# Kernel optimization log

Measured on AMD Instinct MI355X. Metric: run time of the kernel, lower is better.

## Reference

```python
import jax, jax.numpy as jnp
import numpy as np

B, S, D, H = 2, 4096, 1024, 16
DH = D // H  # 64


def setup_inputs() -> dict:
    key = jax.random.key(0)
    ks = jax.random.split(key, 5)
    x = jax.random.normal(ks[0], (B, S, D), dtype=jnp.float32)
    scale = 1.0 / np.sqrt(D)
    Wq = jax.random.normal(ks[1], (D, D), dtype=jnp.float32) * scale
    Wk = jax.random.normal(ks[2], (D, D), dtype=jnp.float32) * scale
    Wv = jax.random.normal(ks[3], (D, D), dtype=jnp.float32) * scale
    Wo = jax.random.normal(ks[4], (D, D), dtype=jnp.float32) * scale
    bo = jnp.zeros((D,), dtype=jnp.float32)
    return {"x": x, "Wq": Wq, "Wk": Wk, "Wv": Wv, "Wo": Wo, "bo": bo}


def reference(x, Wq, Wk, Wv, Wo, bo):
    b, s, d = x.shape
    # QKV projections (no bias), split heads: [b, s, H, DH]
    q = (x @ Wq).reshape(b, s, H, DH)
    k = (x @ Wk).reshape(b, s, H, DH)
    v = (x @ Wv).reshape(b, s, H, DH)
    # scores: [b, H, s, s]
    scores = jnp.einsum("bqhd,bkhd->bhqk", q, k)
    # causal mask: upper triangle (j > i) set to -inf, then scale by sqrt(d_head)
    causal = jnp.triu(jnp.ones((s, s), dtype=bool), k=1)
    scores = jnp.where(causal, -jnp.inf, scores)
    weights = jax.nn.softmax(scores / jnp.sqrt(jnp.float32(DH)), axis=-1)
    # dropout rate is 0.0 -> identity
    ctx = jnp.einsum("bhqk,bkhd->bqhd", weights, v).reshape(b, s, d)
    return ctx @ Wo + bo
```

## Files before the change

### kernel.cpp

```cpp
#include <hip/hip_runtime.h>
#include <hip/hip_bf16.h>
#include <stdint.h>
#include <math.h>

#define BATCH 2
#define S_LEN 4096
#define DMODEL 1024
#define NH 16
#define DHEAD 64
#define MTOK (BATCH * S_LEN)

#define QSCALE 0.1803368801111793f

typedef unsigned short u16;
typedef __attribute__((ext_vector_type(8))) short bf16x8;
typedef __attribute__((ext_vector_type(4))) float f32x4;
typedef __attribute__((ext_vector_type(16))) float f32x16;
typedef __attribute__((ext_vector_type(4))) unsigned short u16x4;

__device__ __forceinline__ float b2f(u16 u) {
  union { unsigned int i; float f; } v; v.i = ((unsigned int)u) << 16; return v.f;
}
__device__ __forceinline__ u16 f2b(float f) {
  union { float f; unsigned int i; } v; v.f = f;
  unsigned int r = v.i + 0x7FFF + ((v.i >> 16) & 1);
  return (u16)(r >> 16);
}
__device__ __forceinline__ unsigned int pk2(float hi, float lo) {
  union { float f; unsigned int u; } a, b; a.f = hi; b.f = lo;
  return __builtin_amdgcn_perm(a.u, b.u, 0x07060302u);
}
__device__ __forceinline__ void pswap(unsigned int& a, unsigned int& b) {
  asm("v_permlane32_swap_b32 %0, %1" : "+v"(a), "+v"(b));
}

__device__ __forceinline__ void gl_lds16(const u16* g, u16* l) {
  __builtin_amdgcn_global_load_lds(
      (__attribute__((address_space(1))) void*)(u16*)g,
      (__attribute__((address_space(3))) void*)l, 16, 0, 0);
}

__global__ void detect_dtype(const unsigned int* __restrict__ x, int* __restrict__ flag) {
  __shared__ int cnt;
  if (threadIdx.x == 0) cnt = 0;
  __syncthreads();
  int c = 0;
  for (int i = threadIdx.x; i < 4096; i += 256) {
    unsigned int w = x[i];
    int e = (w >> 7) & 0xFF;
    if (e >= 100 && e <= 135) c++;
  }
  atomicAdd(&cnt, c);
  __syncthreads();
  if (threadIdx.x == 0) *flag = (cnt > 2048) ? 1 : 0;
}

__global__ void convert_x(const void* __restrict__ xin, u16* __restrict__ xc,
                          const int* __restrict__ flagp) {
  const int isb = *flagp;
  long e = ((long)blockIdx.x * 256 + threadIdx.x) * 4;
  if (isb) {
    *(uint2*)&xc[e] = *(const uint2*)((const u16*)xin + e);
  } else {
    float4 f = *(const float4*)((const float*)xin + e);
    xc[e + 0] = f2b(f.x);
    xc[e + 1] = f2b(f.y);
    xc[e + 2] = f2b(f.z);
    xc[e + 3] = f2b(f.w);
  }
}

__global__ void transpose4(const void* __restrict__ W0, const void* __restrict__ W1,
                           const void* __restrict__ W2, const void* __restrict__ W3,
                           u16* __restrict__ out, const int* __restrict__ flagp) {
  __shared__ u16 tile[32][33];
  const int isb = *flagp;
  int z = blockIdx.z;
  const void* W = (z == 0) ? W0 : (z == 1) ? W1 : (z == 2) ? W2 : W3;
  u16* o = out + (long)z * (DMODEL * DMODEL);
  int x = blockIdx.x * 32 + threadIdx.x;
  int y0 = blockIdx.y * 32;
  if (isb) {
    const u16* Wb = (const u16*)W;
#pragma unroll
    for (int i = 0; i < 32; i += 8)
      tile[threadIdx.y + i][threadIdx.x] = Wb[(long)(y0 + threadIdx.y + i) * DMODEL + x];
  } else {
    const float* Wf = (const float*)W;
#pragma unroll
    for (int i = 0; i < 32; i += 8)
      tile[threadIdx.y + i][threadIdx.x] = f2b(Wf[(long)(y0 + threadIdx.y + i) * DMODEL + x]);
  }
  __syncthreads();
  int x2 = blockIdx.y * 32 + threadIdx.x;
  int y2 = blockIdx.x * 32;
#pragma unroll
  for (int i = 0; i < 32; i += 8)
    o[(long)(y2 + threadIdx.y + i) * DMODEL + x2] = tile[threadIdx.x][threadIdx.y + i];
}

#define BM 128
#define BN 128
#define BK 32

#define GEMM_CORE(A_, Bt_, Kd_)                                                   \
  __shared__ __align__(16) u16 lA[BM * BK];                                       \
  __shared__ __align__(16) u16 lB[BN * BK];                                       \
  const int tid = threadIdx.x;                                                    \
  const int w = tid >> 6;                                                         \
  const int lane = tid & 63;                                                      \
  const int m0 = blockIdx.y * BM;                                                 \
  const int n0 = blockIdx.x * BN;                                                 \
  const int wm = (w >> 1) * 64;                                                   \
  const int wn = (w & 1) * 64;                                                    \
  const int lc = lane & 15;                                                       \
  const int lq = lane >> 4;                                                       \
  f32x4 acc[4][4] = {};                                                           \
  for (int k0 = 0; k0 < (Kd_); k0 += BK) {                                        \
    __syncthreads();                                                              \
    _Pragma("unroll")                                                             \
    for (int jj = 0; jj < 2; ++jj) {                                              \
      int base = (jj * 4 + w) * 512;                                              \
      int e = base + lane * 8;                                                    \
      int row = e >> 5, col = e & 31;                                             \
      gl_lds16((A_) + (long)(m0 + row) * (Kd_) + k0 + col, lA + base);            \
      gl_lds16((Bt_) + (long)(n0 + row) * (Kd_) + k0 + col, lB + base);           \
    }                                                                             \
    __syncthreads();                                                              \
    bf16x8 af[4], bg[4];                                                          \
    _Pragma("unroll")                                                             \
    for (int i = 0; i < 4; ++i)                                                   \
      af[i] = *(const bf16x8*)&lA[(wm + i * 16 + lc) * BK + lq * 8];              \
    _Pragma("unroll")                                                             \
    for (int j = 0; j < 4; ++j)                                                   \
      bg[j] = *(const bf16x8*)&lB[(wn + j * 16 + lc) * BK + lq * 8];              \
    _Pragma("unroll")                                                             \
    for (int i = 0; i < 4; ++i)                                                   \
      _Pragma("unroll")                                                           \
      for (int j = 0; j < 4; ++j)                                                 \
        acc[i][j] = __builtin_amdgcn_mfma_f32_16x16x32_bf16(af[i], bg[j], acc[i][j], 0, 0, 0); \
  }

__global__ __launch_bounds__(256)
void gemm_qkv(const u16* __restrict__ A, const u16* __restrict__ Bt,
              u16* __restrict__ Qo, u16* __restrict__ Ko, u16* __restrict__ Vo) {
  GEMM_CORE(A, Bt, DMODEL)
#pragma unroll
  for (int i = 0; i < 4; ++i) {
#pragma unroll
    for (int j = 0; j < 4; ++j) {
      int n = n0 + wn + j * 16 + lc;
      int rgn = n >> 10;
      int nn = n & 1023;
      int h = nn >> 6, dh = nn & (DHEAD - 1);
      float sc = (rgn == 0) ? QSCALE : 1.0f;
#pragma unroll
      for (int r = 0; r < 4; ++r) {
        int m = m0 + wm + i * 16 + lq * 4 + r;
        int b = m >> 12, s = m & (S_LEN - 1);
        float v = acc[i][j][r] * sc;
        long idx_r = (((long)(b * NH + h)) * S_LEN + s) * DHEAD + dh;
        long idx_v = (((long)(b * NH + h)) * DHEAD + dh) * S_LEN + s;
        if (rgn == 0)      Qo[idx_r] = f2b(v);
        else if (rgn == 1) Ko[idx_r] = f2b(v);
        else               Vo[idx_v] = f2b(v);
      }
    }
  }
}

__global__ __launch_bounds__(256)
void gemm_out(const u16* __restrict__ A, const u16* __restrict__ Bt,
              const void* __restrict__ bias, void* __restrict__ C,
              const int* __restrict__ flagp) {
  GEMM_CORE(A, Bt, DMODEL)
  const int isb = *flagp;
#pragma unroll
  for (int i = 0; i < 4; ++i) {
#pragma unroll
    for (int j = 0; j < 4; ++j) {
      int n = n0 + wn + j * 16 + lc;
      float bv = isb ? b2f(((const u16*)bias)[n]) : ((const float*)bias)[n];
#pragma unroll
      for (int r = 0; r < 4; ++r) {
        int m = m0 + wm + i * 16 + lq * 4 + r;
        float v = acc[i][j][r] + bv;
        if (isb) ((u16*)C)[(long)m * DMODEL + n] = f2b(v);
        else     ((float*)C)[(long)m * DMODEL + n] = v;
      }
    }
  }
}

__global__ __launch_bounds__(256, 2)
void flash_attn(const u16* __restrict__ Q, const u16* __restrict__ K,
                const u16* __restrict__ Vt, u16* __restrict__ ctx) {
  __shared__ __align__(16) u16 lK[64 * 64];
  __shared__ __align__(16) u16 lV[64 * 64];

  const int tid = threadIdx.x;
  const int w = tid >> 6;
  const int lane = tid & 63;
  const int l31 = lane & 31;
  const int l5 = lane >> 5;

  const int hb = blockIdx.x;
  const int h = hb & (NH - 1);
  const int b = hb >> 4;
  const int qt = gridDim.y - 1 - (int)blockIdx.y;
  const int q0 = qt * 128;

  const int bh = b * NH + h;
  const u16* Qb = Q + (long)bh * S_LEN * DHEAD;
  const u16* Kb = K + (long)bh * S_LEN * DHEAD;
  const u16* Vb = Vt + (long)bh * DHEAD * S_LEN;

  const int qa = q0 + w * 32;
  const int myq = qa + l31;

  bf16x8 aq[4];
#pragma unroll
  for (int c = 0; c < 4; ++c)
    aq[c] = *(const bf16x8*)(Qb + (long)myq * DHEAD + c * 16 + l5 * 8);

  const int srow = tid >> 2;
  const int sc0 = (tid & 3) * 2;
  const int sd0 = srow * 64 + ((sc0 ^ (srow & 7)) * 8);
  const int sd1 = srow * 64 + (((sc0 + 1) ^ (srow & 7)) * 8);
  const u16* kp = Kb + (long)srow * DHEAD + sc0 * 8;
  const u16* vp = Vb + (long)srow * S_LEN + sc0 * 8;

  const int kmax = q0 + 64;
  bf16x8 kr0 = *(const bf16x8*)kp;
  bf16x8 kr1 = *(const bf16x8*)(kp + 8);
  bf16x8 vr0 = *(const bf16x8*)vp;
  bf16x8 vr1 = *(const bf16x8*)(vp + 8);

  f32x16 o0 = {}, o1 = {};
  float lsum = 0.0f;
  const int xsw = l31 & 7;

  for (int k0 = 0; k0 <= kmax; k0 += 64) {
    *(bf16x8*)&lK[sd0] = kr0;
    *(bf16x8*)&lK[sd1] = kr1;
    *(bf16x8*)&lV[sd0] = vr0;
    *(bf16x8*)&lV[sd1] = vr1;
    __syncthreads();

    if (k0 + 64 <= kmax) {
      kr0 = *(const bf16x8*)(kp + (long)(k0 + 64) * DHEAD);
      kr1 = *(const bf16x8*)(kp + (long)(k0 + 64) * DHEAD + 8);
      vr0 = *(const bf16x8*)(vp + k0 + 64);
      vr1 = *(const bf16x8*)(vp + k0 + 64 + 8);
    }

    if (k0 <= qa + 31) {
      f32x16 s0 = {}, s1 = {};
#pragma unroll
      for (int c = 0; c < 4; ++c) {
        const int ch = c * 2 + l5;
        bf16x8 ak0 = *(const bf16x8*)&lK[l31 * 64 + ((ch ^ xsw) * 8)];
        bf16x8 ak1 = *(const bf16x8*)&lK[(32 + l31) * 64 + ((ch ^ xsw) * 8)];
        s0 = __builtin_amdgcn_mfma_f32_32x32x16_bf16(ak0, aq[c], s0, 0, 0, 0);
        s1 = __builtin_amdgcn_mfma_f32_32x32x16_bf16(ak1, aq[c], s1, 0, 0, 0);
      }

      const bool masked = (k0 + 63 > qa);
      union BPU { unsigned int wd[4]; bf16x8 v; };
      BPU bp[4];
      float ls = 0.0f;
#pragma unroll
      for (int ph = 0; ph < 2; ++ph) {
        const f32x16 sv = ph ? s1 : s0;
        float p[16];
#pragma unroll
        for (int rr = 0; rr < 16; ++rr) {
          float e = exp2f(sv[rr]);
          if (masked) {
            int kv = k0 + ph * 32 + (rr & 3) + 8 * (rr >> 2) + 4 * l5;
            e = (kv > myq) ? 0.0f : e;
          }
          p[rr] = e;
          ls += e;
        }
#pragma unroll
        for (int g = 0; g < 2; ++g) {
          unsigned int A0 = pk2(p[8 * g + 1], p[8 * g + 0]);
          unsigned int A1 = pk2(p[8 * g + 3], p[8 * g + 2]);
          unsigned int B0 = pk2(p[8 * g + 5], p[8 * g + 4]);
          unsigned int B1 = pk2(p[8 * g + 7], p[8 * g + 6]);
          pswap(A0, B0);
          pswap(A1, B1);
          const int kc = ph * 2 + g;
          bp[kc].wd[0] = A0; bp[kc].wd[1] = A1;
          bp[kc].wd[2] = B0; bp[kc].wd[3] = B1;
        }
      }
      lsum += ls;

#pragma unroll
      for (int kc = 0; kc < 4; ++kc) {
        const int ch = kc * 2 + l5;
        bf16x8 av0 = *(const bf16x8*)&lV[l31 * 64 + ((ch ^ xsw) * 8)];
        bf16x8 av1 = *(const bf16x8*)&lV[(32 + l31) * 64 + ((ch ^ xsw) * 8)];
        o0 = __builtin_amdgcn_mfma_f32_32x32x16_bf16(av0, bp[kc].v, o0, 0, 0, 0);
        o1 = __builtin_amdgcn_mfma_f32_32x32x16_bf16(av1, bp[kc].v, o1, 0, 0, 0);
      }
    }
    __syncthreads();
  }

  lsum += __shfl_xor(lsum, 32, 64);
  float inv = 1.0f / lsum;

  u16* cp = ctx + ((long)(b * S_LEN + myq)) * DMODEL + h * DHEAD;
#pragma unroll
  for (int d32 = 0; d32 < 2; ++d32) {
    const f32x16 ov = d32 ? o1 : o0;
#pragma unroll
    for (int g = 0; g < 4; ++g) {
      u16x4 st;
#pragma unroll
      for (int r = 0; r < 4; ++r) st[r] = f2b(ov[4 * g + r] * inv);
      *(u16x4*)&cp[d32 * 32 + g * 8 + l5 * 4] = st;
    }
  }
}

extern "C" void kernel_launch(void* const* d_in, const int* in_sizes, int n_in,
                              void* d_out, int out_size, void* d_ws, size_t ws_size,
                              hipStream_t stream) {
  const void* x  = d_in[0];
  const void* Wq = d_in[1];
  const void* Wk = d_in[2];
  const void* Wv = d_in[3];
  const void* Wo = d_in[4];
  const void* bo = d_in[5];
  u16* ws = (u16*)d_ws;

  u16* wt  = ws;
  u16* wto = wt + 3145728;
  u16* Qb  = ws + 4194304;
  u16* Vtb = ws + 12582912;
  u16* xc  = ws + 20971520;
  u16* ctx = xc;
  int* flag = (int*)(ws + 29360128);
  u16* Kb  = (u16*)d_out;

  detect_dtype<<<1, 256, 0, stream>>>((const unsigned int*)x, flag);
  convert_x<<<8192, 256, 0, stream>>>(x, xc, flag);
  transpose4<<<dim3(32, 32, 4), dim3(32, 8), 0, stream>>>(Wq, Wk, Wv, Wo, wt, flag);

  gemm_qkv<<<dim3(3 * DMODEL / BN, MTOK / BM), 256, 0, stream>>>(xc, wt, Qb, Kb, Vtb);

  flash_attn<<<dim3(NH * BATCH, S_LEN / 128), 256, 0, stream>>>(Qb, Kb, Vtb, ctx);

  gemm_out<<<dim3(DMODEL / BN, MTOK / BM), 256, 0, stream>>>(ctx, wto, bo, d_out, flag);
}
```

Measured before the change: 346.4 us.

## Compute softmax row sums via MFMA with ones matrix, add setprio and precomputed offsets

The per-lane scalar accumulation of exponentials is replaced by an extra MFMA that multiplies a bf16 ones matrix by the probability tile, so the row sums come out of the matrix unit and the cross-lane shuffle is no longer needed. It also precomputes the swizzled LDS offsets and uses incrementing prefetch pointers. Wave priority is raised around the MFMA blocks, and exp2f is swapped for the hardware exp2 builtin. Summing the bf16-rounded probabilities keeps the normalizer consistent with the PV product, but it adds a third MFMA per chunk and a 16-register accumulator.

```diff
diff --git a/kernel.cpp b/kernel.cpp
--- a/kernel.cpp
+++ b/kernel.cpp
@@ -223,6 +223,10 @@
   for (int c = 0; c < 4; ++c)
     aq[c] = *(const bf16x8*)(Qb + (long)myq * DHEAD + c * 16 + l5 * 8);
 
+  union OU { unsigned int wd[4]; bf16x8 v; } ones;
+#pragma unroll
+  for (int i = 0; i < 4; ++i) ones.wd[i] = 0x3F803F80u;
+
   const int srow = tid >> 2;
   const int sc0 = (tid & 3) * 2;
   const int sd0 = srow * 64 + ((sc0 ^ (srow & 7)) * 8);
@@ -235,10 +239,22 @@
   bf16x8 kr1 = *(const bf16x8*)(kp + 8);
   bf16x8 vr0 = *(const bf16x8*)vp;
   bf16x8 vr1 = *(const bf16x8*)(vp + 8);
+  const u16* kpre = kp + 64 * DHEAD;
+  const u16* vpre = vp + 64;
 
   f32x16 o0 = {}, o1 = {};
-  float lsum = 0.0f;
+  f32x16 lacc = {};
   const int xsw = l31 & 7;
+
+  int offK[4][2], offV[4][2];
+#pragma unroll
+  for (int c = 0; c < 4; ++c) {
+    const int ch = c * 2 + l5;
+    offK[c][0] = l31 * 64 + ((ch ^ xsw) * 8);
+    offK[c][1] = (32 + l31) * 64 + ((ch ^ xsw) * 8);
+    offV[c][0] = offK[c][0];
+    offV[c][1] = offK[c][1];
+  }
 
   for (int k0 = 0; k0 <= kmax; k0 += 64) {
     *(bf16x8*)&lK[sd0] = kr0;
@@ -248,40 +264,41 @@
     __syncthreads();
 
     if (k0 + 64 <= kmax) {
-      kr0 = *(const bf16x8*)(kp + (long)(k0 + 64) * DHEAD);
-      kr1 = *(const bf16x8*)(kp + (long)(k0 + 64) * DHEAD + 8);
-      vr0 = *(const bf16x8*)(vp + k0 + 64);
-      vr1 = *(const bf16x8*)(vp + k0 + 64 + 8);
+      kr0 = *(const bf16x8*)kpre;
+      kr1 = *(const bf16x8*)(kpre + 8);
+      vr0 = *(const bf16x8*)vpre;
+      vr1 = *(const bf16x8*)(vpre + 8);
+      kpre += 64 * DHEAD;
+      vpre += 64;
     }
 
     if (k0 <= qa + 31) {
       f32x16 s0 = {}, s1 = {};
+      __builtin_amdgcn_s_setprio(1);
 #pragma unroll
       for (int c = 0; c < 4; ++c) {
-        const int ch = c * 2 + l5;
-        bf16x8 ak0 = *(const bf16x8*)&lK[l31 * 64 + ((ch ^ xsw) * 8)];
-        bf16x8 ak1 = *(const bf16x8*)&lK[(32 + l31) * 64 + ((ch ^ xsw) * 8)];
+        bf16x8 ak0 = *(const bf16x8*)&lK[offK[c][0]];
+        bf16x8 ak1 = *(const bf16x8*)&lK[offK[c][1]];
         s0 = __builtin_amdgcn_mfma_f32_32x32x16_bf16(ak0, aq[c], s0, 0, 0, 0);
         s1 = __builtin_amdgcn_mfma_f32_32x32x16_bf16(ak1, aq[c], s1, 0, 0, 0);
       }
+      __builtin_amdgcn_s_setprio(0);
 
       const bool masked = (k0 + 63 > qa);
       union BPU { unsigned int wd[4]; bf16x8 v; };
       BPU bp[4];
-      float ls = 0.0f;
 #pragma unroll
       for (int ph = 0; ph < 2; ++ph) {
         const f32x16 sv = ph ? s1 : s0;
         float p[16];
 #pragma unroll
         for (int rr = 0; rr < 16; ++rr) {
-          float e = exp2f(sv[rr]);
+          float e = __builtin_amdgcn_exp2f(sv[rr]);
           if (masked) {
             int kv = k0 + ph * 32 + (rr & 3) + 8 * (rr >> 2) + 4 * l5;
             e = (kv > myq) ? 0.0f : e;
           }
           p[rr] = e;
-          ls += e;
         }
 #pragma unroll
         for (int g = 0; g < 2; ++g) {
@@ -296,22 +313,22 @@
           bp[kc].wd[2] = B0; bp[kc].wd[3] = B1;
         }
       }
-      lsum += ls;
-
+
+      __builtin_amdgcn_s_setprio(1);
 #pragma unroll
       for (int kc = 0; kc < 4; ++kc) {
-        const int ch = kc * 2 + l5;
-        bf16x8 av0 = *(const bf16x8*)&lV[l31 * 64 + ((ch ^ xsw) * 8)];
-        bf16x8 av1 = *(const bf16x8*)&lV[(32 + l31) * 64 + ((ch ^ xsw) * 8)];
+        bf16x8 av0 = *(const bf16x8*)&lV[offV[kc][0]];
+        bf16x8 av1 = *(const bf16x8*)&lV[offV[kc][1]];
         o0 = __builtin_amdgcn_mfma_f32_32x32x16_bf16(av0, bp[kc].v, o0, 0, 0, 0);
         o1 = __builtin_amdgcn_mfma_f32_32x32x16_bf16(av1, bp[kc].v, o1, 0, 0, 0);
-      }
+        lacc = __builtin_amdgcn_mfma_f32_32x32x16_bf16(ones.v, bp[kc].v, lacc, 0, 0, 0);
+      }
+      __builtin_amdgcn_s_setprio(0);
     }
     __syncthreads();
   }
 
-  lsum += __shfl_xor(lsum, 32, 64);
-  float inv = 1.0f / lsum;
+  float inv = 1.0f / lacc[0];
 
   u16* cp = ctx + ((long)(b * S_LEN + myq)) * DMODEL + h * DHEAD;
 #pragma unroll
```

New measurement: 318.2 us. -8.2%, faster.
